# Optimization experiments

Hardware: AMD Instinct MI355X
Metric: run time of the kernel (lower is better)

## Reference

```python
import jax, jax.numpy as jnp
import numpy as np

CAP_FACTOR = 1.25


def _moe_top1(x, wg, w1, b1, w2, b2):
    """Top-1 switch MoE with capacity-based token dropping.
    x: [T, d]; wg: [d, E]; w1: [E, d, f]; b1: [E, f]; w2: [E, f, d]; b2: [E, d].
    """
    T, d = x.shape
    E = wg.shape[1]
    cap = int(CAP_FACTOR * T / E)
    probs = jax.nn.softmax(x @ wg, axis=-1)            # [T, E]
    idx = jnp.argmax(probs, axis=-1)                   # [T] expert assignment
    gate = jnp.max(probs, axis=-1)                     # [T] gate prob
    oh = jax.nn.one_hot(idx, E, dtype=jnp.int32)       # [T, E]
    # position of each token within its expert's buffer
    pos = (jnp.cumsum(oh, axis=0) * oh).sum(-1) - 1    # [T]
    keep = pos < cap                                   # drop tokens over capacity
    pos_w = jnp.where(keep, pos, cap)                  # dropped -> overflow slot
    # dispatch: scatter tokens into per-expert buffers [E, cap+1, d]
    buf = jnp.zeros((E, cap + 1, d), dtype=x.dtype).at[idx, pos_w].set(x)
    buf = buf[:, :cap]                                 # slice off overflow slot
    # grouped expert FFN
    h = jax.nn.relu(jnp.einsum('ecd,edf->ecf', buf, w1) + b1[:, None, :])
    eo = jnp.einsum('ecf,efd->ecd', h, w2) + b2[:, None, :]
    # combine: gather each token's expert output, scale by gate prob, zero dropped
    pos_g = jnp.minimum(pos_w, cap - 1)
    out = eo[idx, pos_g] * (gate * keep.astype(x.dtype))[:, None]
    return out


def setup_inputs():
    key = jax.random.key(0)
    ks = jax.random.split(key, 12)
    B, S, d, dff, E1, E2 = 8, 2048, 1024, 4096, 8, 16
    s = lambda fan: np.float32(1.0 / np.sqrt(fan))
    return dict(
        x=jax.random.normal(ks[0], (B, S, d), jnp.float32),
        y=jax.random.randint(ks[1], (B,), 0, d),
        wg1=jax.random.normal(ks[2], (d, E1), jnp.float32) * s(d),
        w1a=jax.random.normal(ks[3], (E1, d, dff), jnp.float32) * s(d),
        b1a=jnp.zeros((E1, dff), jnp.float32),
        w2a=jax.random.normal(ks[4], (E1, dff, d), jnp.float32) * s(dff),
        b2a=jnp.zeros((E1, d), jnp.float32),
        wg2=jax.random.normal(ks[5], (d, E2), jnp.float32) * s(d),
        w1b=jax.random.normal(ks[6], (E2, d, dff), jnp.float32) * s(d),
        b1b=jnp.zeros((E2, dff), jnp.float32),
        w2b=jax.random.normal(ks[7], (E2, dff, d), jnp.float32) * s(dff),
        b2b=jnp.zeros((E2, d), jnp.float32),
    )


def reference(x, y, wg1, w1a, b1a, w2a, b2a, wg2, w1b, b1b, w2b, b2b):
    B, S, d = x.shape
    xf = x.reshape(B * S, d)
    m1 = _moe_top1(xf, wg1, w1a, b1a, w2a, b2a)        # moe1(x)
    m2 = _moe_top1(m1, wg2, w1b, b1b, w2b, b2b)        # moe2(moe_out)
    resid = x + m2.reshape(B, S, d)                    # residual add
    sent = resid.mean(axis=1)                          # [B, d] mean-pool -> logits
    logp = jax.nn.log_softmax(sent, axis=-1)
    return -logp[jnp.arange(B), y].mean()              # cross-entropy loss
```

## Files before the change

### kernel.cpp

```cpp
#include <hip/hip_runtime.h>
#include <hip/hip_bf16.h>
#include <cstdint>
#include <cstddef>

#define B_    8
#define S_    2048
#define D_    1024
#define DFF_  4096
#define E1_   8
#define E2_   16
#define T_    (B_*S_)
#define CAP1_ 2560
#define CAP2_ 1280
#define EC_   20480

typedef __bf16 bf16x8 __attribute__((ext_vector_type(8)));
typedef float  f32x4  __attribute__((ext_vector_type(4)));

__device__ __forceinline__ unsigned short f2bf(float x) {
  return __builtin_bit_cast(unsigned short, (__bf16)x);
}

template<int E>
__global__ __launch_bounds__(256)
void gate_kernel(const float* __restrict__ X, const float* __restrict__ WG,
                 int* __restrict__ idxO, float* __restrict__ gateO) {
  const int lane = threadIdx.x & 63;
  const int wv   = threadIdx.x >> 6;
  const int t    = blockIdx.x * 4 + wv;
  const float* xr = X + (size_t)t * D_;
  float acc[E];
#pragma unroll
  for (int e = 0; e < E; ++e) acc[e] = 0.f;
#pragma unroll
  for (int i = 0; i < 4; ++i) {
    float4 xv = *(const float4*)(xr + i * 256 + lane * 4);
    int kb = i * 256 + lane * 4;
#pragma unroll
    for (int j = 0; j < 4; ++j) {
      float xs = (&xv.x)[j];
      const float* wr = WG + (size_t)(kb + j) * E;
#pragma unroll
      for (int e = 0; e < E; ++e) acc[e] += xs * wr[e];
    }
  }
#pragma unroll
  for (int e = 0; e < E; ++e) {
    float v = acc[e];
#pragma unroll
    for (int s = 32; s >= 1; s >>= 1) v += __shfl_xor(v, s, 64);
    acc[e] = v;
  }
  if (lane == 0) {
    float mx = acc[0]; int mi = 0;
#pragma unroll
    for (int e = 1; e < E; ++e) if (acc[e] > mx) { mx = acc[e]; mi = e; }
    float s = 0.f;
#pragma unroll
    for (int e = 0; e < E; ++e) s += expf(acc[e] - mx);
    idxO[t]  = mi;
    gateO[t] = 1.0f / s;
  }
}

__global__ __launch_bounds__(1024)
void scan_kernel(const int* __restrict__ idx, int E, int cap,
                 int* __restrict__ pos, int* __restrict__ kept) {
  __shared__ int cnt[16][17];
  __shared__ int gbase[16];
  const int tid = threadIdx.x;
  const int w = tid >> 6, lane = tid & 63;
  if (tid < E) gbase[tid] = 0;
  __syncthreads();
  const unsigned long long lt = (lane == 63) ? 0xFFFFFFFFFFFFFFFFull >> 1
                                             : ((1ull << lane) - 1ull);
  for (int it = 0; it < T_ / 1024; ++it) {
    int t = it * 1024 + tid;
    int mi = idx[t];
    int rank = 0;
    for (int e = 0; e < E; ++e) {
      unsigned long long m = __ballot(mi == e);
      if (lane == 0) cnt[w][e] = __popcll(m);
      if (mi == e) rank = __popcll(m & lt);
    }
    __syncthreads();
    int off = 0;
    for (int w2 = 0; w2 < w; ++w2) off += cnt[w2][mi];
    pos[t] = gbase[mi] + off + rank;
    __syncthreads();
    if (tid < E) {
      int tot = 0;
      for (int w2 = 0; w2 < 16; ++w2) tot += cnt[w2][tid];
      gbase[tid] += tot;
    }
    __syncthreads();
  }
  if (tid < E) kept[tid] = min(gbase[tid], cap);
}

__global__ __launch_bounds__(64)
void scatter_kernel(const float* __restrict__ X, const int* __restrict__ idx,
                    const int* __restrict__ pos, int cap,
                    unsigned short* __restrict__ xbuf, int* __restrict__ tokmap,
                    float* __restrict__ mzero) {
  const int t = blockIdx.x;
  const int lane = threadIdx.x;
  const int p = pos[t];
  if (p < cap) {
    const size_t dst = ((size_t)idx[t] * cap + p) * D_;
    const float* xr = X + (size_t)t * D_;
#pragma unroll
    for (int i = 0; i < 4; ++i) {
      float4 v = *(const float4*)(xr + i * 256 + lane * 4);
      ushort4 o;
      o.x = f2bf(v.x); o.y = f2bf(v.y); o.z = f2bf(v.z); o.w = f2bf(v.w);
      *(ushort4*)(xbuf + dst + i * 256 + lane * 4) = o;
    }
    if (lane == 0) tokmap[(size_t)idx[t] * cap + p] = t;
  } else {
    float4 z = {0.f, 0.f, 0.f, 0.f};
    float* mr = mzero + (size_t)t * D_;
#pragma unroll
    for (int i = 0; i < 4; ++i) *(float4*)(mr + i * 256 + lane * 4) = z;
  }
}

__global__ __launch_bounds__(256)
void wtrans_kernel(const float* __restrict__ src, unsigned short* __restrict__ dst,
                   int K, int N) {
  __shared__ float t[64][65];
  const int tid = threadIdx.x;
  const size_t eo = (size_t)blockIdx.z * K * N;
  const int k0 = blockIdx.y * 64, n0 = blockIdx.x * 64;
  const float* s = src + eo + (size_t)k0 * N + n0;
  unsigned short* d = dst + eo + (size_t)n0 * K + k0;
#pragma unroll
  for (int i = 0; i < 4; ++i) {
    int k = i * 16 + (tid >> 4);
    int n4 = (tid & 15) * 4;
    float4 v = *(const float4*)(s + (size_t)k * N + n4);
    t[k][n4] = v.x; t[k][n4 + 1] = v.y; t[k][n4 + 2] = v.z; t[k][n4 + 3] = v.w;
  }
  __syncthreads();
#pragma unroll
  for (int i = 0; i < 4; ++i) {
    int n = i * 16 + (tid >> 4);
    int k4 = (tid & 15) * 4;
    ushort4 o;
    o.x = f2bf(t[k4][n]);     o.y = f2bf(t[k4 + 1][n]);
    o.z = f2bf(t[k4 + 2][n]); o.w = f2bf(t[k4 + 3][n]);
    *(ushort4*)(d + (size_t)n * K + k4) = o;
  }
}

template<int MODE>
__global__ __launch_bounds__(256, 2)
void moe_gemm(const unsigned short* __restrict__ A,
              const unsigned short* __restrict__ BT,
              const float* __restrict__ bias, int K, int N, int cap, int nbcnt,
              const int* __restrict__ kept,
              unsigned short* __restrict__ Hout, float* __restrict__ Mout,
              const int* __restrict__ tokmap, const float* __restrict__ gate) {
  __shared__ char smem[65536];
  const int tid  = threadIdx.x;
  const int lane = tid & 63;
  const int wv   = tid >> 6;
  const int wr   = wv >> 1, wc = wv & 1;

  const int nwg = gridDim.x;
  const int wg  = (blockIdx.x & 7) * (nwg >> 3) + (blockIdx.x >> 3);
  const int per_grp = nbcnt * 4;
  const int grp = wg / per_grp;
  const int rem = wg - grp * per_grp;
  const int mb  = grp * 4 + (rem & 3);
  const int nb  = rem >> 2;

  const int e  = (mb * 128) / cap;
  const int r0 = mb * 128 - e * cap;
  const int kept_e = kept[e];
  if (r0 >= kept_e) return;
  const unsigned short* Ab = A + (size_t)(mb * 128) * K;
  const unsigned short* Bb = BT + ((size_t)e * N + (size_t)nb * 128) * K;

  f32x4 acc[4][4];
#pragma unroll
  for (int m = 0; m < 4; ++m)
#pragma unroll
    for (int n = 0; n < 4; ++n) acc[m][n] = (f32x4){0.f, 0.f, 0.f, 0.f};

  auto stage = [&](int buf, int k0) {
#pragma unroll
    for (int j = 0; j < 4; ++j) {
      const int c   = j * 256 + tid;
      const int row = c >> 3;
      const int cc  = c & 7;
      const int scol = (cc ^ (row & 7)) << 3;
      const unsigned short* ga = Ab + (size_t)row * K + k0 + scol;
      const unsigned short* gb = Bb + (size_t)row * K + k0 + scol;
      char* la = smem + buf * 32768 + (j * 256 + (tid & ~63)) * 16;
      char* lb = la + 16384;
      __builtin_amdgcn_global_load_lds((const __attribute__((address_space(1))) void*)ga,
                                       (__attribute__((address_space(3))) void*)la,
                                       16, 0, 0);
      __builtin_amdgcn_global_load_lds((const __attribute__((address_space(1))) void*)gb,
                                       (__attribute__((address_space(3))) void*)lb,
                                       16, 0, 0);
    }
  };

  const int NT = K >> 6;
  stage(0, 0);
  __syncthreads();
  int cur = 0;

  const int g16 = (lane >> 4) * 16;
  const int r16 = lane & 15;

  for (int t = 0; t < NT; ++t) {
    if (t + 1 < NT) stage(cur ^ 1, (t + 1) << 6);

    const char* As = smem + cur * 32768;
    const char* Bs = As + 16384;
    bf16x8 af[4][2], bfr[4][2];
#pragma unroll
    for (int m = 0; m < 4; ++m) {
      const int row = wr * 64 + m * 16 + r16;
      const int sw  = (row & 7) << 4;
#pragma unroll
      for (int ks = 0; ks < 2; ++ks)
        af[m][ks] = *(const bf16x8*)(As + row * 128 + ((ks * 64 + g16) ^ sw));
    }
#pragma unroll
    for (int n = 0; n < 4; ++n) {
      const int row = wc * 64 + n * 16 + r16;
      const int sw  = (row & 7) << 4;
#pragma unroll
      for (int ks = 0; ks < 2; ++ks)
        bfr[n][ks] = *(const bf16x8*)(Bs + row * 128 + ((ks * 64 + g16) ^ sw));
    }
    __builtin_amdgcn_s_setprio(1);
#pragma unroll
    for (int ks = 0; ks < 2; ++ks)
#pragma unroll
      for (int m = 0; m < 4; ++m)
#pragma unroll
        for (int n = 0; n < 4; ++n)
          acc[m][n] = __builtin_amdgcn_mfma_f32_16x16x32_bf16(af[m][ks], bfr[n][ks], acc[m][n], 0, 0, 0);
    __builtin_amdgcn_s_setprio(0);
    __syncthreads();
    cur ^= 1;
  }

  const int rg = lane >> 4;
  float bv[4];
#pragma unroll
  for (int n = 0; n < 4; ++n)
    bv[n] = bias[(size_t)e * N + nb * 128 + wc * 64 + n * 16 + r16];

#pragma unroll
  for (int m = 0; m < 4; ++m) {
#pragma unroll
    for (int r = 0; r < 4; ++r) {
      const int lrow = wr * 64 + m * 16 + rg * 4 + r;
      if (MODE == 0) {
        unsigned short* orow = Hout + (size_t)(mb * 128 + lrow) * N + nb * 128;
#pragma unroll
        for (int n = 0; n < 4; ++n) {
          float v = acc[m][n][r] + bv[n];
          orow[wc * 64 + n * 16 + r16] = f2bf(fmaxf(v, 0.f));
        }
      } else {
        const int lr = r0 + lrow;
        if (lr < kept_e) {
          const int tok = tokmap[mb * 128 + lrow];
          const float gsc = gate[tok];
          float* orow = Mout + (size_t)tok * N + nb * 128;
#pragma unroll
          for (int n = 0; n < 4; ++n)
            orow[wc * 64 + n * 16 + r16] = (acc[m][n][r] + bv[n]) * gsc;
        }
      }
    }
  }
}

__global__ __launch_bounds__(256)
void reduce_kernel(const float* __restrict__ X, const float* __restrict__ M2,
                   float* __restrict__ sent) {
  const int c = blockIdx.x * 256 + threadIdx.x;
  const int b = blockIdx.z;
  const int s0 = blockIdx.y * 128;
  float a = 0.f;
  size_t base = ((size_t)b * S_ + s0) * D_ + c;
  for (int s = 0; s < 128; ++s) a += X[base + (size_t)s * D_] + M2[base + (size_t)s * D_];
  atomicAdd(&sent[b * D_ + c], a * (1.0f / (float)S_));
}

__global__ __launch_bounds__(64)
void loss_kernel(const float* __restrict__ sent, const int* __restrict__ y,
                 float* __restrict__ out) {
  const int lane = threadIdx.x;
  float total = 0.f;
  for (int b = 0; b < B_; ++b) {
    const float* s = sent + b * D_;
    float v[16];
    float mx = -1e30f;
#pragma unroll
    for (int i = 0; i < 16; ++i) { v[i] = s[lane + i * 64]; mx = fmaxf(mx, v[i]); }
#pragma unroll
    for (int sh = 32; sh >= 1; sh >>= 1) mx = fmaxf(mx, __shfl_xor(mx, sh, 64));
    float sm = 0.f;
#pragma unroll
    for (int i = 0; i < 16; ++i) sm += expf(v[i] - mx);
#pragma unroll
    for (int sh = 32; sh >= 1; sh >>= 1) sm += __shfl_xor(sm, sh, 64);
    total += logf(sm) + mx - s[y[b]];
  }
  if (lane == 0) out[0] = total * (1.0f / (float)B_);
}

extern "C" void kernel_launch(void* const* d_in, const int* in_sizes, int n_in,
                              void* d_out, int out_size, void* d_ws, size_t ws_size,
                              hipStream_t stream) {
  const float* x   = (const float*)d_in[0];
  const int*   y   = (const int*)d_in[1];
  const float* wg1 = (const float*)d_in[2];
  const float* w1a = (const float*)d_in[3];
  const float* b1a = (const float*)d_in[4];
  const float* w2a = (const float*)d_in[5];
  const float* b2a = (const float*)d_in[6];
  const float* wg2 = (const float*)d_in[7];
  const float* w1b = (const float*)d_in[8];
  const float* b1b = (const float*)d_in[9];
  const float* w2b = (const float*)d_in[10];
  const float* b2b = (const float*)d_in[11];
  float* out = (float*)d_out;
  (void)in_sizes; (void)n_in; (void)out_size; (void)ws_size;

  char* base = (char*)d_ws;
  size_t o = 0;
  auto alloc = [&](size_t bytes) { size_t r = o; o = (o + bytes + 255) & ~(size_t)255; return r; };
  int*   idx1    = (int*)  (base + alloc((size_t)T_ * 4));
  int*   pos1    = (int*)  (base + alloc((size_t)T_ * 4));
  float* gate1   = (float*)(base + alloc((size_t)T_ * 4));
  int*   idx2    = (int*)  (base + alloc((size_t)T_ * 4));
  int*   pos2    = (int*)  (base + alloc((size_t)T_ * 4));
  float* gate2   = (float*)(base + alloc((size_t)T_ * 4));
  int*   kept1   = (int*)  (base + alloc(64 * 4));
  int*   kept2   = (int*)  (base + alloc(64 * 4));
  int*   tokmap1 = (int*)  (base + alloc((size_t)EC_ * 4));
  int*   tokmap2 = (int*)  (base + alloc((size_t)EC_ * 4));
  float* sent    = (float*)(base + alloc((size_t)B_ * D_ * 4));
  float* m1      = (float*)(base + alloc((size_t)T_ * D_ * 4));
  unsigned short* xbuf = (unsigned short*)(base + alloc((size_t)EC_ * D_ * 2));
  unsigned short* h    = (unsigned short*)(base + alloc((size_t)EC_ * DFF_ * 2));
  unsigned short* wT   = (unsigned short*)(base + alloc((size_t)E2_ * D_ * DFF_ * 2));

  hipMemsetAsync(sent, 0, (size_t)B_ * D_ * 4, stream);

  gate_kernel<E1_><<<T_ / 4, 256, 0, stream>>>(x, wg1, idx1, gate1);
  scan_kernel<<<1, 1024, 0, stream>>>(idx1, E1_, CAP1_, pos1, kept1);
  scatter_kernel<<<T_, 64, 0, stream>>>(x, idx1, pos1, CAP1_, xbuf, tokmap1, m1);
  wtrans_kernel<<<dim3(DFF_ / 64, D_ / 64, E1_), 256, 0, stream>>>(w1a, wT, D_, DFF_);
  moe_gemm<0><<<(DFF_ / 128) * (EC_ / 128), 256, 0, stream>>>(
      xbuf, wT, b1a, D_, DFF_, CAP1_, DFF_ / 128, kept1, h, nullptr, nullptr, nullptr);
  wtrans_kernel<<<dim3(D_ / 64, DFF_ / 64, E1_), 256, 0, stream>>>(w2a, wT, DFF_, D_);
  moe_gemm<1><<<(D_ / 128) * (EC_ / 128), 256, 0, stream>>>(
      h, wT, b2a, DFF_, D_, CAP1_, D_ / 128, kept1, nullptr, m1, tokmap1, gate1);

  gate_kernel<E2_><<<T_ / 4, 256, 0, stream>>>(m1, wg2, idx2, gate2);
  scan_kernel<<<1, 1024, 0, stream>>>(idx2, E2_, CAP2_, pos2, kept2);
  scatter_kernel<<<T_, 64, 0, stream>>>(m1, idx2, pos2, CAP2_, xbuf, tokmap2, m1);
  wtrans_kernel<<<dim3(DFF_ / 64, D_ / 64, E2_), 256, 0, stream>>>(w1b, wT, D_, DFF_);
  moe_gemm<0><<<(DFF_ / 128) * (EC_ / 128), 256, 0, stream>>>(
      xbuf, wT, b1b, D_, DFF_, CAP2_, DFF_ / 128, kept2, h, nullptr, nullptr, nullptr);
  wtrans_kernel<<<dim3(D_ / 64, DFF_ / 64, E2_), 256, 0, stream>>>(w2b, wT, DFF_, D_);
  moe_gemm<1><<<(D_ / 128) * (EC_ / 128), 256, 0, stream>>>(
      h, wT, b2b, DFF_, D_, CAP2_, D_ / 128, kept2, nullptr, m1, tokmap2, gate2);

  reduce_kernel<<<dim3(D_ / 256, S_ / 128, B_), 256, 0, stream>>>(x, m1, sent);
  loss_kernel<<<1, 64, 0, stream>>>(sent, y, out);
}
```

Before: 1.381 ms.

## Fuse weight transpose and bf16 conversion into MoE GEMM B-tile loading

Drops the four separate weight transpose kernels. The GEMM now reads the fp32 expert weights directly in register-staged strided loads, converts them to bf16 and writes them transposed into swizzled LDS. The B loads for the next tile are issued before the MFMA work and written to LDS after it, to overlap with compute. The block-to-tile swizzle group also widens from 4 to 8 M-blocks to improve weight reuse in L2. The cost is twice the global weight bytes per tile, scalar strided global loads, extra registers for the staging buffer, and an explicit vmcnt(0) wait each iteration.

```diff
diff --git a/kernel.cpp b/kernel.cpp
--- a/kernel.cpp
+++ b/kernel.cpp
@@ -20,6 +20,9 @@
 __device__ __forceinline__ unsigned short f2bf(float x) {
   return __builtin_bit_cast(unsigned short, (__bf16)x);
 }
+
+#define SB0 __builtin_amdgcn_sched_barrier(0)
+#define VM0 asm volatile("s_waitcnt vmcnt(0)" ::: "memory")
 
 template<int E>
 __global__ __launch_bounds__(256)
@@ -125,38 +128,10 @@
   }
 }
 
-__global__ __launch_bounds__(256)
-void wtrans_kernel(const float* __restrict__ src, unsigned short* __restrict__ dst,
-                   int K, int N) {
-  __shared__ float t[64][65];
-  const int tid = threadIdx.x;
-  const size_t eo = (size_t)blockIdx.z * K * N;
-  const int k0 = blockIdx.y * 64, n0 = blockIdx.x * 64;
-  const float* s = src + eo + (size_t)k0 * N + n0;
-  unsigned short* d = dst + eo + (size_t)n0 * K + k0;
-#pragma unroll
-  for (int i = 0; i < 4; ++i) {
-    int k = i * 16 + (tid >> 4);
-    int n4 = (tid & 15) * 4;
-    float4 v = *(const float4*)(s + (size_t)k * N + n4);
-    t[k][n4] = v.x; t[k][n4 + 1] = v.y; t[k][n4 + 2] = v.z; t[k][n4 + 3] = v.w;
-  }
-  __syncthreads();
-#pragma unroll
-  for (int i = 0; i < 4; ++i) {
-    int n = i * 16 + (tid >> 4);
-    int k4 = (tid & 15) * 4;
-    ushort4 o;
-    o.x = f2bf(t[k4][n]);     o.y = f2bf(t[k4 + 1][n]);
-    o.z = f2bf(t[k4 + 2][n]); o.w = f2bf(t[k4 + 3][n]);
-    *(ushort4*)(d + (size_t)n * K + k4) = o;
-  }
-}
-
 template<int MODE>
 __global__ __launch_bounds__(256, 2)
 void moe_gemm(const unsigned short* __restrict__ A,
-              const unsigned short* __restrict__ BT,
+              const float* __restrict__ Bw,
               const float* __restrict__ bias, int K, int N, int cap, int nbcnt,
               const int* __restrict__ kept,
               unsigned short* __restrict__ Hout, float* __restrict__ Mout,
@@ -169,18 +144,18 @@
 
   const int nwg = gridDim.x;
   const int wg  = (blockIdx.x & 7) * (nwg >> 3) + (blockIdx.x >> 3);
-  const int per_grp = nbcnt * 4;
+  const int per_grp = nbcnt * 8;
   const int grp = wg / per_grp;
   const int rem = wg - grp * per_grp;
-  const int mb  = grp * 4 + (rem & 3);
-  const int nb  = rem >> 2;
+  const int mb  = grp * 8 + (rem & 7);
+  const int nb  = rem >> 3;
 
   const int e  = (mb * 128) / cap;
   const int r0 = mb * 128 - e * cap;
   const int kept_e = kept[e];
   if (r0 >= kept_e) return;
   const unsigned short* Ab = A + (size_t)(mb * 128) * K;
-  const unsigned short* Bb = BT + ((size_t)e * N + (size_t)nb * 128) * K;
+  const float* Bb = Bw + (size_t)e * K * N + (size_t)nb * 128;
 
   f32x4 acc[4][4];
 #pragma unroll
@@ -188,37 +163,68 @@
 #pragma unroll
     for (int n = 0; n < 4; ++n) acc[m][n] = (f32x4){0.f, 0.f, 0.f, 0.f};
 
-  auto stage = [&](int buf, int k0) {
+  size_t boff[4]; int bswz[4];
+#pragma unroll
+  for (int j = 0; j < 4; ++j) {
+    const int c  = j * 256 + tid;
+    const int n  = c & 127;
+    const int k8 = c >> 7;
+    boff[j] = (size_t)(k8 * 8) * N + n;
+    bswz[j] = 16384 + n * 128 + ((k8 * 16) ^ ((n & 7) << 4));
+  }
+  float bq[4][8];
+
+  auto stageA = [&](int buf, int k0) {
 #pragma unroll
     for (int j = 0; j < 4; ++j) {
       const int c   = j * 256 + tid;
       const int row = c >> 3;
-      const int cc  = c & 7;
-      const int scol = (cc ^ (row & 7)) << 3;
+      const int scol = ((c & 7) ^ (row & 7)) * 8;
       const unsigned short* ga = Ab + (size_t)row * K + k0 + scol;
-      const unsigned short* gb = Bb + (size_t)row * K + k0 + scol;
       char* la = smem + buf * 32768 + (j * 256 + (tid & ~63)) * 16;
-      char* lb = la + 16384;
       __builtin_amdgcn_global_load_lds((const __attribute__((address_space(1))) void*)ga,
                                        (__attribute__((address_space(3))) void*)la,
                                        16, 0, 0);
-      __builtin_amdgcn_global_load_lds((const __attribute__((address_space(1))) void*)gb,
-                                       (__attribute__((address_space(3))) void*)lb,
-                                       16, 0, 0);
     }
   };
+  auto loadB = [&](int k0) {
+    const float* p = Bb + (size_t)k0 * N;
+#pragma unroll
+    for (int j = 0; j < 4; ++j)
+#pragma unroll
+      for (int i = 0; i < 8; ++i)
+        bq[j][i] = p[boff[j] + (size_t)i * N];
+  };
+  auto writeB = [&](int buf) {
+#pragma unroll
+    for (int j = 0; j < 4; ++j) {
+      uint4 pk;
+      unsigned int* pw = (unsigned int*)&pk;
+#pragma unroll
+      for (int q = 0; q < 4; ++q)
+        pw[q] = (unsigned int)f2bf(bq[j][2 * q]) |
+                ((unsigned int)f2bf(bq[j][2 * q + 1]) << 16);
+      *(uint4*)(smem + buf * 32768 + bswz[j]) = pk;
+    }
+  };
 
   const int NT = K >> 6;
-  stage(0, 0);
+  stageA(0, 0);
+  loadB(0);
+  VM0; SB0;
+  writeB(0);
   __syncthreads();
-  int cur = 0;
 
   const int g16 = (lane >> 4) * 16;
   const int r16 = lane & 15;
+  int cur = 0;
 
   for (int t = 0; t < NT; ++t) {
-    if (t + 1 < NT) stage(cur ^ 1, (t + 1) << 6);
-
+    if (t + 1 < NT) {
+      stageA(cur ^ 1, (t + 1) << 6);
+      loadB((t + 1) << 6);
+      SB0;
+    }
     const char* As = smem + cur * 32768;
     const char* Bs = As + 16384;
     bf16x8 af[4][2], bfr[4][2];
@@ -247,6 +253,10 @@
         for (int n = 0; n < 4; ++n)
           acc[m][n] = __builtin_amdgcn_mfma_f32_16x16x32_bf16(af[m][ks], bfr[n][ks], acc[m][n], 0, 0, 0);
     __builtin_amdgcn_s_setprio(0);
+    if (t + 1 < NT) {
+      VM0; SB0;
+      writeB(cur ^ 1);
+    }
     __syncthreads();
     cur ^= 1;
   }
@@ -354,29 +364,24 @@
   float* m1      = (float*)(base + alloc((size_t)T_ * D_ * 4));
   unsigned short* xbuf = (unsigned short*)(base + alloc((size_t)EC_ * D_ * 2));
   unsigned short* h    = (unsigned short*)(base + alloc((size_t)EC_ * DFF_ * 2));
-  unsigned short* wT   = (unsigned short*)(base + alloc((size_t)E2_ * D_ * DFF_ * 2));
 
   hipMemsetAsync(sent, 0, (size_t)B_ * D_ * 4, stream);
 
   gate_kernel<E1_><<<T_ / 4, 256, 0, stream>>>(x, wg1, idx1, gate1);
   scan_kernel<<<1, 1024, 0, stream>>>(idx1, E1_, CAP1_, pos1, kept1);
   scatter_kernel<<<T_, 64, 0, stream>>>(x, idx1, pos1, CAP1_, xbuf, tokmap1, m1);
-  wtrans_kernel<<<dim3(DFF_ / 64, D_ / 64, E1_), 256, 0, stream>>>(w1a, wT, D_, DFF_);
   moe_gemm<0><<<(DFF_ / 128) * (EC_ / 128), 256, 0, stream>>>(
-      xbuf, wT, b1a, D_, DFF_, CAP1_, DFF_ / 128, kept1, h, nullptr, nullptr, nullptr);
-  wtrans_kernel<<<dim3(D_ / 64, DFF_ / 64, E1_), 256, 0, stream>>>(w2a, wT, DFF_, D_);
+      xbuf, w1a, b1a, D_, DFF_, CAP1_, DFF_ / 128, kept1, h, nullptr, nullptr, nullptr);
   moe_gemm<1><<<(D_ / 128) * (EC_ / 128), 256, 0, stream>>>(
-      h, wT, b2a, DFF_, D_, CAP1_, D_ / 128, kept1, nullptr, m1, tokmap1, gate1);
+      h, w2a, b2a, DFF_, D_, CAP1_, D_ / 128, kept1, nullptr, m1, tokmap1, gate1);
 
   gate_kernel<E2_><<<T_ / 4, 256, 0, stream>>>(m1, wg2, idx2, gate2);
   scan_kernel<<<1, 1024, 0, stream>>>(idx2, E2_, CAP2_, pos2, kept2);
   scatter_kernel<<<T_, 64, 0, stream>>>(m1, idx2, pos2, CAP2_, xbuf, tokmap2, m1);
-  wtrans_kernel<<<dim3(DFF_ / 64, D_ / 64, E2_), 256, 0, stream>>>(w1b, wT, D_, DFF_);
   moe_gemm<0><<<(DFF_ / 128) * (EC_ / 128), 256, 0, stream>>>(
-      xbuf, wT, b1b, D_, DFF_, CAP2_, DFF_ / 128, kept2, h, nullptr, nullptr, nullptr);
-  wtrans_kernel<<<dim3(D_ / 64, DFF_ / 64, E2_), 256, 0, stream>>>(w2b, wT, DFF_, D_);
+      xbuf, w1b, b1b, D_, DFF_, CAP2_, DFF_ / 128, kept2, h, nullptr, nullptr, nullptr);
   moe_gemm<1><<<(D_ / 128) * (EC_ / 128), 256, 0, stream>>>(
-      h, wT, b2b, DFF_, D_, CAP2_, D_ / 128, kept2, nullptr, m1, tokmap2, gate2);
+      h, w2b, b2b, DFF_, D_, CAP2_, D_ / 128, kept2, nullptr, m1, tokmap2, gate2);
 
   reduce_kernel<<<dim3(D_ / 256, S_ / 128, B_), 256, 0, stream>>>(x, m1, sent);
   loss_kernel<<<1, 64, 0, stream>>>(sent, y, out);
```

Result: slower. 1.546 ms (+11.9%).

## Fold next weight transpose into preceding MoE GEMM blocks and widen M grouping

Applied to the files above, without the earlier changes.

Each grouped GEMM launch now also transposes and converts the next GEMM's fp32 weights to bf16 tiles at block start, into a second ping-pong buffer. This removes separate transpose launches and overlaps that memory-bound work with the GEMM, including blocks that would otherwise exit early for dropped rows. It falls back to the old sequence if the workspace is too small. The block-to-tile swizzle also groups 8 M-blocks instead of 4 to improve L2 reuse of weights. The cost is a prologue in every GEMM block, an extra sync, and a second weight buffer.

```diff
diff --git a/kernel.cpp b/kernel.cpp
--- a/kernel.cpp
+++ b/kernel.cpp
@@ -20,6 +20,9 @@
 __device__ __forceinline__ unsigned short f2bf(float x) {
   return __builtin_bit_cast(unsigned short, (__bf16)x);
 }
+
+#define SB0 __builtin_amdgcn_sched_barrier(0)
+#define VM0 asm volatile("s_waitcnt vmcnt(0)" ::: "memory")
 
 template<int E>
 __global__ __launch_bounds__(256)
@@ -160,20 +163,55 @@
               const float* __restrict__ bias, int K, int N, int cap, int nbcnt,
               const int* __restrict__ kept,
               unsigned short* __restrict__ Hout, float* __restrict__ Mout,
-              const int* __restrict__ tokmap, const float* __restrict__ gate) {
+              const int* __restrict__ tokmap, const float* __restrict__ gate,
+              const float* __restrict__ tsrc, unsigned short* __restrict__ tdst,
+              int tK, int tN, int tE, int tpb) {
   __shared__ char smem[65536];
   const int tid  = threadIdx.x;
+
+  if (tsrc != nullptr) {
+    float (*tt)[65] = (float(*)[65])smem;
+    const int ntn = tN >> 6, ntk = tK >> 6;
+    const int tiles = tE * ntk * ntn;
+    int t0 = blockIdx.x * tpb;
+    int t1 = t0 + tpb; if (t1 > tiles) t1 = tiles;
+    for (int t = t0; t < t1; ++t) {
+      const int e2 = t / (ntk * ntn), rem = t - e2 * (ntk * ntn);
+      const int k0 = (rem / ntn) << 6, n0 = (rem - (rem / ntn) * ntn) << 6;
+      const float* s = tsrc + (size_t)e2 * tK * tN + (size_t)k0 * tN + n0;
+      unsigned short* d2 = tdst + (size_t)e2 * tK * tN + (size_t)n0 * tK + k0;
+#pragma unroll
+      for (int i = 0; i < 4; ++i) {
+        int k = i * 16 + (tid >> 4);
+        int n4 = (tid & 15) * 4;
+        float4 v = *(const float4*)(s + (size_t)k * tN + n4);
+        tt[k][n4] = v.x; tt[k][n4 + 1] = v.y; tt[k][n4 + 2] = v.z; tt[k][n4 + 3] = v.w;
+      }
+      __syncthreads();
+#pragma unroll
+      for (int i = 0; i < 4; ++i) {
+        int n = i * 16 + (tid >> 4);
+        int k4 = (tid & 15) * 4;
+        ushort4 o;
+        o.x = f2bf(tt[k4][n]);     o.y = f2bf(tt[k4 + 1][n]);
+        o.z = f2bf(tt[k4 + 2][n]); o.w = f2bf(tt[k4 + 3][n]);
+        *(ushort4*)(d2 + (size_t)n * tK + k4) = o;
+      }
+      __syncthreads();
+    }
+  }
+
   const int lane = tid & 63;
   const int wv   = tid >> 6;
   const int wr   = wv >> 1, wc = wv & 1;
 
   const int nwg = gridDim.x;
   const int wg  = (blockIdx.x & 7) * (nwg >> 3) + (blockIdx.x >> 3);
-  const int per_grp = nbcnt * 4;
+  const int per_grp = nbcnt * 8;
   const int grp = wg / per_grp;
   const int rem = wg - grp * per_grp;
-  const int mb  = grp * 4 + (rem & 3);
-  const int nb  = rem >> 2;
+  const int mb  = grp * 8 + (rem & 7);
+  const int nb  = rem >> 3;
 
   const int e  = (mb * 128) / cap;
   const int r0 = mb * 128 - e * cap;
@@ -209,6 +247,7 @@
   };
 
   const int NT = K >> 6;
+  __syncthreads();
   stage(0, 0);
   __syncthreads();
   int cur = 0;
@@ -335,7 +374,7 @@
   const float* w2b = (const float*)d_in[10];
   const float* b2b = (const float*)d_in[11];
   float* out = (float*)d_out;
-  (void)in_sizes; (void)n_in; (void)out_size; (void)ws_size;
+  (void)in_sizes; (void)n_in; (void)out_size;
 
   char* base = (char*)d_ws;
   size_t o = 0;
@@ -354,29 +393,53 @@
   float* m1      = (float*)(base + alloc((size_t)T_ * D_ * 4));
   unsigned short* xbuf = (unsigned short*)(base + alloc((size_t)EC_ * D_ * 2));
   unsigned short* h    = (unsigned short*)(base + alloc((size_t)EC_ * DFF_ * 2));
-  unsigned short* wT   = (unsigned short*)(base + alloc((size_t)E2_ * D_ * DFF_ * 2));
+  unsigned short* P1   = (unsigned short*)(base + alloc((size_t)E2_ * D_ * DFF_ * 2));
+  size_t need_with_P2 = o + (size_t)E2_ * D_ * DFF_ * 2 + 256;
+  const bool fold = (ws_size >= need_with_P2);
+  unsigned short* P2 = fold ? (unsigned short*)(base + alloc((size_t)E2_ * D_ * DFF_ * 2))
+                            : P1;
 
   hipMemsetAsync(sent, 0, (size_t)B_ * D_ * 4, stream);
+
+  const int G0 = (DFF_ / 128) * (EC_ / 128);
+  const int G1 = (D_  / 128) * (EC_ / 128);
+  const int TPB0 = (8192  + G0 - 1) / G0;
+  const int TPB1 = (16384 + G1 - 1) / G1;
+  const int TPB2 = (16384 + G0 - 1) / G0;
 
   gate_kernel<E1_><<<T_ / 4, 256, 0, stream>>>(x, wg1, idx1, gate1);
   scan_kernel<<<1, 1024, 0, stream>>>(idx1, E1_, CAP1_, pos1, kept1);
   scatter_kernel<<<T_, 64, 0, stream>>>(x, idx1, pos1, CAP1_, xbuf, tokmap1, m1);
-  wtrans_kernel<<<dim3(DFF_ / 64, D_ / 64, E1_), 256, 0, stream>>>(w1a, wT, D_, DFF_);
-  moe_gemm<0><<<(DFF_ / 128) * (EC_ / 128), 256, 0, stream>>>(
-      xbuf, wT, b1a, D_, DFF_, CAP1_, DFF_ / 128, kept1, h, nullptr, nullptr, nullptr);
-  wtrans_kernel<<<dim3(D_ / 64, DFF_ / 64, E1_), 256, 0, stream>>>(w2a, wT, DFF_, D_);
-  moe_gemm<1><<<(D_ / 128) * (EC_ / 128), 256, 0, stream>>>(
-      h, wT, b2a, DFF_, D_, CAP1_, D_ / 128, kept1, nullptr, m1, tokmap1, gate1);
+  wtrans_kernel<<<dim3(DFF_ / 64, D_ / 64, E1_), 256, 0, stream>>>(w1a, P1, D_, DFF_);
+  if (fold) {
+    moe_gemm<0><<<G0, 256, 0, stream>>>(xbuf, P1, b1a, D_, DFF_, CAP1_, DFF_ / 128,
+        kept1, h, nullptr, nullptr, nullptr, w2a, P2, DFF_, D_, E1_, TPB0);
+    moe_gemm<1><<<G1, 256, 0, stream>>>(h, P2, b2a, DFF_, D_, CAP1_, D_ / 128,
+        kept1, nullptr, m1, tokmap1, gate1, w1b, P1, D_, DFF_, E2_, TPB1);
+  } else {
+    moe_gemm<0><<<G0, 256, 0, stream>>>(xbuf, P1, b1a, D_, DFF_, CAP1_, DFF_ / 128,
+        kept1, h, nullptr, nullptr, nullptr, nullptr, nullptr, 0, 0, 0, 0);
+    wtrans_kernel<<<dim3(D_ / 64, DFF_ / 64, E1_), 256, 0, stream>>>(w2a, P2, DFF_, D_);
+    moe_gemm<1><<<G1, 256, 0, stream>>>(h, P2, b2a, DFF_, D_, CAP1_, D_ / 128,
+        kept1, nullptr, m1, tokmap1, gate1, nullptr, nullptr, 0, 0, 0, 0);
+    wtrans_kernel<<<dim3(DFF_ / 64, D_ / 64, E2_), 256, 0, stream>>>(w1b, P1, D_, DFF_);
+  }
 
   gate_kernel<E2_><<<T_ / 4, 256, 0, stream>>>(m1, wg2, idx2, gate2);
   scan_kernel<<<1, 1024, 0, stream>>>(idx2, E2_, CAP2_, pos2, kept2);
   scatter_kernel<<<T_, 64, 0, stream>>>(m1, idx2, pos2, CAP2_, xbuf, tokmap2, m1);
-  wtrans_kernel<<<dim3(DFF_ / 64, D_ / 64, E2_), 256, 0, stream>>>(w1b, wT, D_, DFF_);
-  moe_gemm<0><<<(DFF_ / 128) * (EC_ / 128), 256, 0, stream>>>(
-      xbuf, wT, b1b, D_, DFF_, CAP2_, DFF_ / 128, kept2, h, nullptr, nullptr, nullptr);
-  wtrans_kernel<<<dim3(D_ / 64, DFF_ / 64, E2_), 256, 0, stream>>>(w2b, wT, DFF_, D_);
-  moe_gemm<1><<<(D_ / 128) * (EC_ / 128), 256, 0, stream>>>(
-      h, wT, b2b, DFF_, D_, CAP2_, D_ / 128, kept2, nullptr, m1, tokmap2, gate2);
+  if (fold) {
+    moe_gemm<0><<<G0, 256, 0, stream>>>(xbuf, P1, b1b, D_, DFF_, CAP2_, DFF_ / 128,
+        kept2, h, nullptr, nullptr, nullptr, w2b, P2, DFF_, D_, E2_, TPB2);
+    moe_gemm<1><<<G1, 256, 0, stream>>>(h, P2, b2b, DFF_, D_, CAP2_, D_ / 128,
+        kept2, nullptr, m1, tokmap2, gate2, nullptr, nullptr, 0, 0, 0, 0);
+  } else {
+    moe_gemm<0><<<G0, 256, 0, stream>>>(xbuf, P1, b1b, D_, DFF_, CAP2_, DFF_ / 128,
+        kept2, h, nullptr, nullptr, nullptr, nullptr, nullptr, 0, 0, 0, 0);
+    wtrans_kernel<<<dim3(D_ / 64, DFF_ / 64, E2_), 256, 0, stream>>>(w2b, P2, DFF_, D_);
+    moe_gemm<1><<<G1, 256, 0, stream>>>(h, P2, b2b, DFF_, D_, CAP2_, D_ / 128,
+        kept2, nullptr, m1, tokmap2, gate2, nullptr, nullptr, 0, 0, 0, 0);
+  }
 
   reduce_kernel<<<dim3(D_ / 256, S_ / 128, B_), 256, 0, stream>>>(x, m1, sent);
   loss_kernel<<<1, 64, 0, stream>>>(sent, y, out);
```

Result: faster. 1.348 ms (-2.4%).
